# Kernel optimization log

Hardware: AMD Instinct MI355X
Metric: run time of the kernel (lower is better)

Reference implementation:

```python
import jax, jax.numpy as jnp
import numpy as np

DIM = 1024
H = 16          # num_heads
D = DIM // H    # head_dim = 64
HID = H * D
N, T = 2, 1024


def setup_inputs() -> dict:
    key = jax.random.key(0)
    ks = jax.random.split(key, 6)
    x = jax.random.normal(ks[0], (N, T, DIM), dtype=jnp.float32)
    # torch nn.Linear stores weight as (out_features, in_features); y = x @ W.T + b
    key_w = jax.random.normal(ks[1], (HID, DIM), dtype=jnp.float32) * DIM ** -0.5
    key_b = jax.random.uniform(ks[2], (HID,), minval=-4.0, maxval=4.0, dtype=jnp.float32)
    vq_w = jax.random.normal(ks[3], (2 * HID, DIM), dtype=jnp.float32) * DIM ** -0.5
    out_w = jax.random.normal(ks[4], (DIM, HID), dtype=jnp.float32) * HID ** -0.5
    out_b = jax.random.normal(ks[5], (DIM,), dtype=jnp.float32) * 0.02
    return {"x": x, "key_w": key_w, "key_b": key_b, "vq_w": vq_w,
            "out_w": out_w, "out_b": out_b}


def reference(x, key_w, key_b, vq_w, out_w, out_b):
    n, t, dim = x.shape
    # projections
    vq = x @ vq_w.T                      # (N,T,2*HID), no bias
    v, q = jnp.split(vq, 2, axis=-1)     # chunk order: v first, q second
    k = jax.nn.sigmoid(x @ key_w.T + key_b)  # (N,T,HID)
    k = k.reshape(n, t, H, D)
    v = v.reshape(n, t, H, D)
    # outer-product update: upd[i,j] = (1-k_i) * v_j  -> (N,T,H,D,D)
    upd = (1.0 - k)[..., :, None] * v[..., None, :]
    # decay per row i is k_i (repeat_interleave over last dim in torch ==
    # broadcasting k over the trailing D axis here)
    decay = k[..., :, None]              # (N,T,H,D,1), broadcasts over j

    # linear recurrence kv_t = decay_t * kv_{t-1} + upd_t via associative scan
    def combine(c1, c2):
        a1, b1 = c1
        a2, b2 = c2
        return (a1 * a2, b1 * a2 + b2)

    _, kv = jax.lax.associative_scan(combine, (decay, upd), axis=1)
    # kv: (N,T,H,D,D)

    qh = q.reshape(n, t, H, D)
    # outer_query_values=False: h = q @ kv, q is (...,1,D) row vector
    h = jnp.einsum('nthd,nthde->nthe', qh, kv).reshape(n, t, HID)
    return h @ out_w.T + out_b
```

## Files before the change

kernel.cpp:

```cpp
#include <hip/hip_runtime.h>
#include <hip/hip_bf16.h>

typedef __attribute__((ext_vector_type(8))) short short8;
typedef __attribute__((ext_vector_type(4))) float f32x4;

constexpr int DIM_ = 1024;
constexpr int H_   = 16;
constexpr int D_   = 64;
constexpr int HID_ = 1024;
constexpr int N_   = 2;
constexpr int T_   = 1024;
constexpr int MTOT = N_ * T_;

constexpr int LC = 32;
constexpr int NC = T_ / LC;
constexpr int NHEAD = N_ * H_;

__device__ __forceinline__ unsigned short f2bf(float f) {
    __hip_bfloat16 h = __float2bfloat16(f);
    unsigned short u; __builtin_memcpy(&u, &h, 2); return u;
}
__device__ __forceinline__ float bf2f(unsigned short u) {
    unsigned int b = ((unsigned int)u) << 16;
    float f; __builtin_memcpy(&f, &b, 4); return f;
}

__device__ __forceinline__ void gload16(const void* g, void* l) {
    __builtin_amdgcn_global_load_lds(
        (const __attribute__((address_space(1))) void*)g,
        (__attribute__((address_space(3))) void*)l, 16, 0, 0);
}

__global__ __launch_bounds__(256) void cvt_all(
    const float* __restrict__ x,  const float* __restrict__ kw,
    const float* __restrict__ vq, const float* __restrict__ ow,
    unsigned short* __restrict__ Xb, unsigned short* __restrict__ Wb,
    unsigned short* __restrict__ OWb)
{
    int b = blockIdx.x;
    const float* src; unsigned short* dst; int off;
    if      (b < 1024) { src = x;  dst = Xb;                 off = b; }
    else if (b < 1536) { src = kw; dst = Wb;                 off = b - 1024; }
    else if (b < 2560) { src = vq; dst = Wb + 1024 * 1024;   off = b - 1536; }
    else               { src = ow; dst = OWb;                off = b - 2560; }
    size_t i = ((size_t)off * 256 + threadIdx.x) * 8;
    float4 v0 = *(const float4*)&src[i];
    float4 v1 = *(const float4*)&src[i + 4];
    short8 o;
    o[0] = (short)f2bf(v0.x); o[1] = (short)f2bf(v0.y);
    o[2] = (short)f2bf(v0.z); o[3] = (short)f2bf(v0.w);
    o[4] = (short)f2bf(v1.x); o[5] = (short)f2bf(v1.y);
    o[6] = (short)f2bf(v1.z); o[7] = (short)f2bf(v1.w);
    *(short8*)&dst[i] = o;
}

#define GEMM_BODY(EPILOGUE)                                                          \
    __shared__ unsigned short As[2][64 * 32];                                        \
    __shared__ unsigned short Bs[2][128 * 32];                                       \
    const int tid = threadIdx.x, w = tid >> 6, lane = tid & 63;                      \
    const int wm = w >> 1, wn = w & 1;                                               \
    const int M0 = blockIdx.y * 64, N0 = blockIdx.x * 128;                           \
    const int srow = tid >> 2;                                                       \
    const int kA = (((tid & 3) ^ ((srow >> 1) & 3)) * 8);                            \
    const unsigned short* gA  = Ab + (size_t)(M0 + srow) * DIM_ + kA;                \
    const unsigned short* gB0 = Bb + (size_t)(N0 + srow) * DIM_ + kA;                \
    const unsigned short* gB1 = Bb + (size_t)(N0 + 64 + srow) * DIM_ + kA;           \
    char* lA0 = (char*)As[0] + w * 1024;                                             \
    char* lA1 = (char*)As[1] + w * 1024;                                             \
    char* lB0 = (char*)Bs[0] + w * 1024;                                             \
    char* lB1 = (char*)Bs[1] + w * 1024;                                             \
    const int fr = lane & 15, fc = lane >> 4;                                        \
    const int p  = fc ^ ((fr >> 1) & 3);                                             \
    const int aoff = (wm * 32 + fr) * 64 + p * 16;                                   \
    const int boff = (wn * 64 + fr) * 64 + p * 16;                                   \
    f32x4 acc[2][4] = {};                                                            \
    for (int k0 = 0; k0 < DIM_; k0 += 64) {                                          \
        __syncthreads();                                                             \
        gload16(gA  + k0,      lA0);                                                 \
        gload16(gA  + k0 + 32, lA1);                                                 \
        gload16(gB0 + k0,      lB0);                                                 \
        gload16(gB1 + k0,      lB0 + 4096);                                          \
        gload16(gB0 + k0 + 32, lB1);                                                 \
        gload16(gB1 + k0 + 32, lB1 + 4096);                                          \
        __syncthreads();                                                             \
        _Pragma("unroll")                                                            \
        for (int half = 0; half < 2; ++half) {                                       \
            short8 a4[2], b4[4];                                                     \
            _Pragma("unroll")                                                        \
            for (int i = 0; i < 2; ++i)                                              \
                a4[i] = *(const short8*)((const char*)As[half] + aoff + i * 1024);   \
            _Pragma("unroll")                                                        \
            for (int i = 0; i < 4; ++i)                                              \
                b4[i] = *(const short8*)((const char*)Bs[half] + boff + i * 1024);   \
            _Pragma("unroll")                                                        \
            for (int mi = 0; mi < 2; ++mi)                                           \
                _Pragma("unroll")                                                    \
                for (int ni = 0; ni < 4; ++ni)                                       \
                    acc[mi][ni] = __builtin_amdgcn_mfma_f32_16x16x32_bf16(           \
                        a4[mi], b4[ni], acc[mi][ni], 0, 0, 0);                       \
        }                                                                            \
    }                                                                                \
    const int cm = M0 + wm * 32 + fc * 4;                                            \
    const int cn = N0 + wn * 64 + fr;                                                \
    EPILOGUE

__global__ __launch_bounds__(256) void gemm_qkv_mfma(
    const unsigned short* __restrict__ Ab,
    const unsigned short* __restrict__ Bb,
    const float* __restrict__ key_b,
    unsigned short* __restrict__ Gb,
    unsigned short* __restrict__ Vb,
    unsigned short* __restrict__ Qb)
{
    GEMM_BODY(
        if (N0 < HID_) {
            _Pragma("unroll")
            for (int ni = 0; ni < 4; ++ni) {
                float bias = key_b[cn + ni * 16];
                _Pragma("unroll")
                for (int mi = 0; mi < 2; ++mi)
                    _Pragma("unroll")
                    for (int r = 0; r < 4; ++r) {
                        float vv = acc[mi][ni][r] + bias;
                        Gb[(size_t)(cm + mi * 16 + r) * HID_ + cn + ni * 16] =
                            f2bf(1.f / (1.f + __expf(vv)));
                    }
            }
        } else if (N0 < 2 * HID_) {
            _Pragma("unroll")
            for (int ni = 0; ni < 4; ++ni)
                _Pragma("unroll")
                for (int mi = 0; mi < 2; ++mi)
                    _Pragma("unroll")
                    for (int r = 0; r < 4; ++r)
                        Vb[(size_t)(cm + mi * 16 + r) * HID_ + cn + ni * 16 - HID_] =
                            f2bf(acc[mi][ni][r]);
        } else {
            _Pragma("unroll")
            for (int ni = 0; ni < 4; ++ni)
                _Pragma("unroll")
                for (int mi = 0; mi < 2; ++mi)
                    _Pragma("unroll")
                    for (int r = 0; r < 4; ++r)
                        Qb[(size_t)(cm + mi * 16 + r) * HID_ + cn + ni * 16 - 2 * HID_] =
                            f2bf(acc[mi][ni][r]);
        }
    )
}

__global__ __launch_bounds__(256) void gemm_out_mfma(
    const unsigned short* __restrict__ Ab,
    const unsigned short* __restrict__ Bb,
    const float* __restrict__ out_b,
    float* __restrict__ Out)
{
    GEMM_BODY(
        _Pragma("unroll")
        for (int ni = 0; ni < 4; ++ni) {
            float bias = out_b[cn + ni * 16];
            _Pragma("unroll")
            for (int mi = 0; mi < 2; ++mi)
                _Pragma("unroll")
                for (int r = 0; r < 4; ++r)
                    Out[(size_t)(cm + mi * 16 + r) * DIM_ + cn + ni * 16] =
                        acc[mi][ni][r] + bias;
        }
    )
}

__global__ __launch_bounds__(256) void scan_phase1(
    const unsigned short* __restrict__ Gb,
    const unsigned short* __restrict__ Vb,
    const unsigned short* __restrict__ Qb,
    unsigned short* __restrict__ SbufB,
    float* __restrict__ Pbuf,
    unsigned short* __restrict__ QAb,
    unsigned short* __restrict__ Hb)
{
    __shared__ float sg[LC][64];
    __shared__ float sv[LC][64];
    __shared__ float sq[LC][64];
    __shared__ unsigned short hp[4][16][64];
    __shared__ unsigned short qs[LC][64];

    const int tid  = threadIdx.x;
    const int w    = tid >> 6;
    const int lane = tid & 63;
    const int c    = blockIdx.x & (NC - 1);
    const int head = blockIdx.x >> 5;
    const int n = head >> 4, h = head & 15;
    const size_t base = ((size_t)n * T_) * HID_ + (size_t)h * 64;

    {
        int f = tid * 8;
        int tl = f >> 6, d = f & 63;
        size_t g = base + (size_t)(c * LC + tl) * HID_ + d;
        short8 g8 = *(const short8*)&Gb[g];
        short8 v8 = *(const short8*)&Vb[g];
        short8 q8 = *(const short8*)&Qb[g];
        #pragma unroll
        for (int j = 0; j < 8; ++j) {
            sg[tl][d + j] = bf2f((unsigned short)g8[j]);
            sv[tl][d + j] = bf2f((unsigned short)v8[j]);
            sq[tl][d + j] = bf2f((unsigned short)q8[j]);
        }
    }
    __syncthreads();

    const int dq = w * 16 + (lane & 15);
    float kv[16];
    #pragma unroll
    for (int i = 0; i < 16; ++i) kv[i] = 0.f;
    float pq = 1.f;

    #pragma unroll
    for (int half = 0; half < 2; ++half) {
        for (int tl2 = 0; tl2 < 16; ++tl2) {
            const int tl = half * 16 + tl2;
            float part = 0.f;
            float v = sv[tl][lane];
            #pragma unroll
            for (int i4 = 0; i4 < 4; ++i4) {
                float4 g4 = *(const float4*)&sg[tl][w * 16 + i4 * 4];
                float4 q4 = *(const float4*)&sq[tl][w * 16 + i4 * 4];
                float gs_[4] = {g4.x, g4.y, g4.z, g4.w};
                float qs_[4] = {q4.x, q4.y, q4.z, q4.w};
                #pragma unroll
                for (int j = 0; j < 4; ++j) {
                    int i = i4 * 4 + j;
                    kv[i] = __builtin_fmaf(gs_[j], v - kv[i], kv[i]);
                    part  = __builtin_fmaf(qs_[j], kv[i], part);
                }
            }
            hp[w][tl2][lane] = f2bf(part);
            pq *= (1.f - sg[tl][dq]);
            if (lane < 16) qs[tl][dq] = f2bf(sq[tl][dq] * pq);
        }
        __syncthreads();
        #pragma unroll
        for (int i = 0; i < 16 * 64 / 256; ++i) {
            int idx = tid + i * 256;
            int tl2 = idx >> 6, e = idx & 63;
            float s = bf2f(hp[0][tl2][e]) + bf2f(hp[1][tl2][e]) +
                      bf2f(hp[2][tl2][e]) + bf2f(hp[3][tl2][e]);
            Hb[base + (size_t)(c * LC + half * 16 + tl2) * HID_ + e] = f2bf(s);
        }
        __syncthreads();
    }

    const size_t sbase = (size_t)(head * NC + c) * (D_ * D_);
    #pragma unroll
    for (int i = 0; i < 4; ++i) {
        ushort4 o = { f2bf(kv[i * 4 + 0]), f2bf(kv[i * 4 + 1]),
                      f2bf(kv[i * 4 + 2]), f2bf(kv[i * 4 + 3]) };
        *(ushort4*)&SbufB[sbase + (size_t)lane * D_ + w * 16 + i * 4] = o;
    }
    if (lane < 16) Pbuf[(size_t)(head * NC + c) * D_ + dq] = pq;
    const unsigned short* qsl = &qs[0][0];
    *(short8*)&QAb[(size_t)(head * NC + c) * (LC * 64) + tid * 8] =
        *(const short8*)&qsl[tid * 8];
}

__global__ __launch_bounds__(256) void scan_combine(
    const unsigned short* __restrict__ SbufB,
    const float* __restrict__ Pbuf,
    unsigned short* __restrict__ SInitB)
{
    const int tid  = threadIdx.x;
    const int head = blockIdx.x >> 4;
    const int e    = (blockIdx.x & 15) * 4 + (tid >> 6);
    const int d    = tid & 63;

    unsigned short Bv[NC];
    float Pv[NC];
    #pragma unroll
    for (int ci = 0; ci < NC; ++ci) {
        const size_t sidx = (size_t)(head * NC + ci) * (D_ * D_) + (size_t)e * D_ + d;
        Bv[ci] = SbufB[sidx];
        Pv[ci] = Pbuf[(size_t)(head * NC + ci) * D_ + d];
    }

    float S = 0.f;
    #pragma unroll
    for (int ci = 0; ci < NC; ++ci) {
        const size_t sidx = (size_t)(head * NC + ci) * (D_ * D_) + (size_t)e * D_ + d;
        SInitB[sidx] = f2bf(S);
        S = Pv[ci] * S + bf2f(Bv[ci]);
    }
}

__global__ __launch_bounds__(256) void scan_inter_mfma(
    const unsigned short* __restrict__ QAb,
    const unsigned short* __restrict__ SInitB,
    unsigned short* __restrict__ Hb)
{
    const int tid = threadIdx.x, w = tid >> 6, lane = tid & 63;
    const int wid  = blockIdx.x * 4 + w;
    const int head = wid >> 5, c = wid & 31;
    if (c == 0) return;
    const int n = head >> 4, h = head & 15;
    const int fr = lane & 15, fc = lane >> 4;

    const unsigned short* qa = QAb + (size_t)(head * NC + c) * (LC * 64);
    const unsigned short* sb = SInitB + (size_t)(head * NC + c) * (D_ * D_);

    short8 a[2][2], b[4][2];
    #pragma unroll
    for (int mi = 0; mi < 2; ++mi)
        #pragma unroll
        for (int ks = 0; ks < 2; ++ks)
            a[mi][ks] = *(const short8*)&qa[(mi * 16 + fr) * 64 + fc * 8 + ks * 32];
    #pragma unroll
    for (int ni = 0; ni < 4; ++ni)
        #pragma unroll
        for (int ks = 0; ks < 2; ++ks)
            b[ni][ks] = *(const short8*)&sb[(ni * 16 + fr) * 64 + fc * 8 + ks * 32];

    f32x4 acc[2][4] = {};
    #pragma unroll
    for (int mi = 0; mi < 2; ++mi)
        #pragma unroll
        for (int ni = 0; ni < 4; ++ni)
            #pragma unroll
            for (int ks = 0; ks < 2; ++ks)
                acc[mi][ni] = __builtin_amdgcn_mfma_f32_16x16x32_bf16(
                    a[mi][ks], b[ni][ks], acc[mi][ni], 0, 0, 0);

    #pragma unroll
    for (int mi = 0; mi < 2; ++mi)
        #pragma unroll
        for (int ni = 0; ni < 4; ++ni)
            #pragma unroll
            for (int r = 0; r < 4; ++r) {
                int t = c * LC + mi * 16 + fc * 4 + r;
                size_t g = ((size_t)n * T_ + t) * HID_ + h * 64 + ni * 16 + fr;
                Hb[g] = f2bf(bf2f(Hb[g]) + acc[mi][ni][r]);
            }
}

extern "C" void kernel_launch(void* const* d_in, const int* in_sizes, int n_in,
                              void* d_out, int out_size, void* d_ws, size_t ws_size,
                              hipStream_t stream)
{
    const float* x     = (const float*)d_in[0];
    const float* key_w = (const float*)d_in[1];
    const float* key_b = (const float*)d_in[2];
    const float* vq_w  = (const float*)d_in[3];
    const float* out_w = (const float*)d_in[4];
    const float* out_b = (const float*)d_in[5];
    float* out = (float*)d_out;

    const size_t MH = (size_t)MTOT * HID_;
    unsigned short* Gb    = (unsigned short*)d_ws;
    unsigned short* Vb16  = Gb + MH;
    unsigned short* Qb16  = Vb16 + MH;
    unsigned short* SbufB = Qb16 + MH;
    unsigned short* SInitB = SbufB + (size_t)NHEAD * NC * D_ * D_;
    float* Pbuf = (float*)(SInitB + (size_t)NHEAD * NC * D_ * D_);
    unsigned short* QAb = (unsigned short*)(Pbuf + (size_t)NHEAD * NC * D_);
    unsigned short* Xb  = QAb + (size_t)NHEAD * NC * LC * D_;
    unsigned short* Wb  = Xb + MH;
    unsigned short* OWb = Wb + 3 * 1024 * 1024;
    unsigned short* Hb  = OWb + 1024 * 1024;

    cvt_all<<<3072, 256, 0, stream>>>(x, key_w, vq_w, out_w, Xb, Wb, OWb);
    gemm_qkv_mfma<<<dim3(24, 32), 256, 0, stream>>>(Xb, Wb, key_b, Gb, Vb16, Qb16);
    scan_phase1<<<NHEAD * NC, 256, 0, stream>>>(Gb, Vb16, Qb16, SbufB, Pbuf, QAb, Hb);
    scan_combine<<<NHEAD * 16, 256, 0, stream>>>(SbufB, Pbuf, SInitB);
    scan_inter_mfma<<<NHEAD * NC / 4, 256, 0, stream>>>(QAb, SInitB, Hb);
    gemm_out_mfma<<<dim3(8, 32), 256, 0, stream>>>(Hb, OWb, out_b, out);
}
```

Baseline: 79.96 us.

## Fuse scan phases into one cooperative kernel with grid syncs

Merges the chunk-local scan, the cross-chunk state combine, and the inter-chunk MFMA correction into a single cooperative kernel separated by grid-wide barriers. The queries stay in swizzled shared memory rather than making a round trip through global memory, and two kernel launches go away. The cost is two grid.sync barriers over 1024 blocks that must all be resident at once, and a combine stage that runs on only 512 blocks while the rest wait. If the cooperative launch fails, the code falls back to the old three-kernel path.

```diff
diff --git a/kernel.cpp b/kernel.cpp
--- a/kernel.cpp
+++ b/kernel.cpp
@@ -1,5 +1,8 @@
 #include <hip/hip_runtime.h>
 #include <hip/hip_bf16.h>
+#include <hip/hip_cooperative_groups.h>
+
+namespace cg = cooperative_groups;
 
 typedef __attribute__((ext_vector_type(8))) short short8;
 typedef __attribute__((ext_vector_type(4))) float f32x4;
@@ -168,13 +171,13 @@
     )
 }
 
-__global__ __launch_bounds__(256) void scan_phase1(
+__global__ __launch_bounds__(256, 4) void scan_fused(
     const unsigned short* __restrict__ Gb,
     const unsigned short* __restrict__ Vb,
     const unsigned short* __restrict__ Qb,
     unsigned short* __restrict__ SbufB,
     float* __restrict__ Pbuf,
-    unsigned short* __restrict__ QAb,
+    unsigned short* __restrict__ SInitB,
     unsigned short* __restrict__ Hb)
 {
     __shared__ float sg[LC][64];
@@ -182,6 +185,8 @@
     __shared__ float sq[LC][64];
     __shared__ unsigned short hp[4][16][64];
     __shared__ unsigned short qs[LC][64];
+
+    cg::grid_group grid = cg::this_grid();
 
     const int tid  = threadIdx.x;
     const int w    = tid >> 6;
@@ -190,6 +195,7 @@
     const int head = blockIdx.x >> 5;
     const int n = head >> 4, h = head & 15;
     const size_t base = ((size_t)n * T_) * HID_ + (size_t)h * 64;
+    const int fr = lane & 15, fc = lane >> 4;
 
     {
         int f = tid * 8;
@@ -234,7 +240,10 @@
             }
             hp[w][tl2][lane] = f2bf(part);
             pq *= (1.f - sg[tl][dq]);
-            if (lane < 16) qs[tl][dq] = f2bf(sq[tl][dq] * pq);
+            if (lane < 16) {
+                int col = ((((dq >> 3) ^ (tl & 7)) << 3) | (dq & 7));
+                qs[tl][col] = f2bf(sq[tl][dq] * pq);
+            }
         }
         __syncthreads();
         #pragma unroll
@@ -256,6 +265,157 @@
         *(ushort4*)&SbufB[sbase + (size_t)lane * D_ + w * 16 + i * 4] = o;
     }
     if (lane < 16) Pbuf[(size_t)(head * NC + c) * D_ + dq] = pq;
+
+    grid.sync();
+
+    if (blockIdx.x < NHEAD * 16) {
+        const int chead = blockIdx.x >> 4;
+        const int ce    = (blockIdx.x & 15) * 4 + (tid >> 6);
+        const int cd    = tid & 63;
+
+        float S = 0.f;
+        for (int cb = 0; cb < NC; cb += 8) {
+            unsigned short Bv[8];
+            float Pv[8];
+            #pragma unroll
+            for (int j = 0; j < 8; ++j) {
+                const size_t sidx = (size_t)(chead * NC + cb + j) * (D_ * D_) + (size_t)ce * D_ + cd;
+                Bv[j] = SbufB[sidx];
+                Pv[j] = Pbuf[(size_t)(chead * NC + cb + j) * D_ + cd];
+            }
+            #pragma unroll
+            for (int j = 0; j < 8; ++j) {
+                const size_t sidx = (size_t)(chead * NC + cb + j) * (D_ * D_) + (size_t)ce * D_ + cd;
+                SInitB[sidx] = f2bf(S);
+                S = Pv[j] * S + bf2f(Bv[j]);
+            }
+        }
+    }
+
+    grid.sync();
+
+    if (c > 0) {
+        const unsigned short* sb = SInitB + (size_t)(head * NC + c) * (D_ * D_);
+        short8 a[2][2], b[2];
+        #pragma unroll
+        for (int mi = 0; mi < 2; ++mi)
+            #pragma unroll
+            for (int ks = 0; ks < 2; ++ks) {
+                int rr = mi * 16 + fr;
+                int byteoff = rr * 128 + (((fc + ks * 4) ^ (rr & 7)) * 16);
+                a[mi][ks] = *(const short8*)((const char*)qs + byteoff);
+            }
+        #pragma unroll
+        for (int ks = 0; ks < 2; ++ks)
+            b[ks] = *(const short8*)&sb[(w * 16 + fr) * 64 + fc * 8 + ks * 32];
+
+        f32x4 acc[2] = {};
+        #pragma unroll
+        for (int mi = 0; mi < 2; ++mi)
+            #pragma unroll
+            for (int ks = 0; ks < 2; ++ks)
+                acc[mi] = __builtin_amdgcn_mfma_f32_16x16x32_bf16(
+                    a[mi][ks], b[ks], acc[mi], 0, 0, 0);
+
+        #pragma unroll
+        for (int mi = 0; mi < 2; ++mi)
+            #pragma unroll
+            for (int r = 0; r < 4; ++r) {
+                int t = c * LC + mi * 16 + fc * 4 + r;
+                size_t g = ((size_t)n * T_ + t) * HID_ + h * 64 + w * 16 + fr;
+                Hb[g] = f2bf(bf2f(Hb[g]) + acc[mi][r]);
+            }
+    }
+}
+
+__global__ __launch_bounds__(256) void scan_phase1(
+    const unsigned short* __restrict__ Gb,
+    const unsigned short* __restrict__ Vb,
+    const unsigned short* __restrict__ Qb,
+    unsigned short* __restrict__ SbufB,
+    float* __restrict__ Pbuf,
+    unsigned short* __restrict__ QAb,
+    unsigned short* __restrict__ Hb)
+{
+    __shared__ float sg[LC][64];
+    __shared__ float sv[LC][64];
+    __shared__ float sq[LC][64];
+    __shared__ unsigned short hp[4][16][64];
+    __shared__ unsigned short qs[LC][64];
+
+    const int tid  = threadIdx.x;
+    const int w    = tid >> 6;
+    const int lane = tid & 63;
+    const int c    = blockIdx.x & (NC - 1);
+    const int head = blockIdx.x >> 5;
+    const int n = head >> 4, h = head & 15;
+    const size_t base = ((size_t)n * T_) * HID_ + (size_t)h * 64;
+
+    {
+        int f = tid * 8;
+        int tl = f >> 6, d = f & 63;
+        size_t g = base + (size_t)(c * LC + tl) * HID_ + d;
+        short8 g8 = *(const short8*)&Gb[g];
+        short8 v8 = *(const short8*)&Vb[g];
+        short8 q8 = *(const short8*)&Qb[g];
+        #pragma unroll
+        for (int j = 0; j < 8; ++j) {
+            sg[tl][d + j] = bf2f((unsigned short)g8[j]);
+            sv[tl][d + j] = bf2f((unsigned short)v8[j]);
+            sq[tl][d + j] = bf2f((unsigned short)q8[j]);
+        }
+    }
+    __syncthreads();
+
+    const int dq = w * 16 + (lane & 15);
+    float kv[16];
+    #pragma unroll
+    for (int i = 0; i < 16; ++i) kv[i] = 0.f;
+    float pq = 1.f;
+
+    #pragma unroll
+    for (int half = 0; half < 2; ++half) {
+        for (int tl2 = 0; tl2 < 16; ++tl2) {
+            const int tl = half * 16 + tl2;
+            float part = 0.f;
+            float v = sv[tl][lane];
+            #pragma unroll
+            for (int i4 = 0; i4 < 4; ++i4) {
+                float4 g4 = *(const float4*)&sg[tl][w * 16 + i4 * 4];
+                float4 q4 = *(const float4*)&sq[tl][w * 16 + i4 * 4];
+                float gs_[4] = {g4.x, g4.y, g4.z, g4.w};
+                float qs_[4] = {q4.x, q4.y, q4.z, q4.w};
+                #pragma unroll
+                for (int j = 0; j < 4; ++j) {
+                    int i = i4 * 4 + j;
+                    kv[i] = __builtin_fmaf(gs_[j], v - kv[i], kv[i]);
+                    part  = __builtin_fmaf(qs_[j], kv[i], part);
+                }
+            }
+            hp[w][tl2][lane] = f2bf(part);
+            pq *= (1.f - sg[tl][dq]);
+            if (lane < 16) qs[tl][dq] = f2bf(sq[tl][dq] * pq);
+        }
+        __syncthreads();
+        #pragma unroll
+        for (int i = 0; i < 16 * 64 / 256; ++i) {
+            int idx = tid + i * 256;
+            int tl2 = idx >> 6, e = idx & 63;
+            float s = bf2f(hp[0][tl2][e]) + bf2f(hp[1][tl2][e]) +
+                      bf2f(hp[2][tl2][e]) + bf2f(hp[3][tl2][e]);
+            Hb[base + (size_t)(c * LC + half * 16 + tl2) * HID_ + e] = f2bf(s);
+        }
+        __syncthreads();
+    }
+
+    const size_t sbase = (size_t)(head * NC + c) * (D_ * D_);
+    #pragma unroll
+    for (int i = 0; i < 4; ++i) {
+        ushort4 o = { f2bf(kv[i * 4 + 0]), f2bf(kv[i * 4 + 1]),
+                      f2bf(kv[i * 4 + 2]), f2bf(kv[i * 4 + 3]) };
+        *(ushort4*)&SbufB[sbase + (size_t)lane * D_ + w * 16 + i * 4] = o;
+    }
+    if (lane < 16) Pbuf[(size_t)(head * NC + c) * D_ + dq] = pq;
     const unsigned short* qsl = &qs[0][0];
     *(short8*)&QAb[(size_t)(head * NC + c) * (LC * 64) + tid * 8] =
         *(const short8*)&qsl[tid * 8];
@@ -279,7 +439,6 @@
         Bv[ci] = SbufB[sidx];
         Pv[ci] = Pbuf[(size_t)(head * NC + ci) * D_ + d];
     }
-
     float S = 0.f;
     #pragma unroll
     for (int ci = 0; ci < NC; ++ci) {
@@ -365,8 +524,17 @@
 
     cvt_all<<<3072, 256, 0, stream>>>(x, key_w, vq_w, out_w, Xb, Wb, OWb);
     gemm_qkv_mfma<<<dim3(24, 32), 256, 0, stream>>>(Xb, Wb, key_b, Gb, Vb16, Qb16);
-    scan_phase1<<<NHEAD * NC, 256, 0, stream>>>(Gb, Vb16, Qb16, SbufB, Pbuf, QAb, Hb);
-    scan_combine<<<NHEAD * 16, 256, 0, stream>>>(SbufB, Pbuf, SInitB);
-    scan_inter_mfma<<<NHEAD * NC / 4, 256, 0, stream>>>(QAb, SInitB, Hb);
+
+    void* args[] = { (void*)&Gb, (void*)&Vb16, (void*)&Qb16,
+                     (void*)&SbufB, (void*)&Pbuf, (void*)&SInitB, (void*)&Hb };
+    hipError_t cerr = hipLaunchCooperativeKernel((const void*)scan_fused,
+                                                 dim3(NHEAD * NC), dim3(256),
+                                                 args, 0, stream);
+    if (cerr != hipSuccess) {
+        scan_phase1<<<NHEAD * NC, 256, 0, stream>>>(Gb, Vb16, Qb16, SbufB, Pbuf, QAb, Hb);
+        scan_combine<<<NHEAD * 16, 256, 0, stream>>>(SbufB, Pbuf, SInitB);
+        scan_inter_mfma<<<NHEAD * NC / 4, 256, 0, stream>>>(QAb, SInitB, Hb);
+    }
+
     gemm_out_mfma<<<dim3(8, 32), 256, 0, stream>>>(Hb, OWb, out_b, out);
 }
```

Result: slower. 291.6 us (+264.7%).
